# Performance work log

Measured on AMD Instinct MI355X. Metric: run time of the kernel, lower is better.

## Reference

```python
import jax, jax.numpy as jnp
import numpy as np


def avg_pool2(x):
    # 2x2 average pool, stride 2, NCHW
    b, c, h, w = x.shape
    return x.reshape(b, c, h // 2, 2, w // 2, 2).mean(axis=(3, 5))


def bisr_conv(x, W, mvk, mvb, beta):
    # ReDistribution: per-channel affine
    x = x * mvk + mvb
    # Spectral binary activation with tanh STE (forward value == sign(x))
    t = jnp.tanh(x * beta)
    xb = jax.lax.stop_gradient(jnp.sign(x)) - jax.lax.stop_gradient(t) + t
    # Binary weights: per-output-channel scale * sign(W), clipped-weight STE
    scale = jnp.mean(jnp.abs(W), axis=(1, 2, 3), keepdims=True)  # [O,1,1,1]
    bw_ng = jax.lax.stop_gradient(scale * jnp.sign(W))
    cw = jnp.clip(W, -1.0, 1.0)
    bw = bw_ng - jax.lax.stop_gradient(cw) + cw
    return jax.lax.conv_general_dilated(
        xb, bw, window_strides=(1, 1), padding=((1, 1), (1, 1)),
        dimension_numbers=('NCHW', 'OIHW', 'NCHW'))


def rprelu(x, pb0, alpha, pb1):
    x = x + pb0
    x = jnp.where(x >= 0, x, alpha * x)  # per-channel PReLU
    return x + pb1


def setup_inputs() -> dict:
    key = jax.random.key(0)
    B, C, H, W = 16, 128, 128, 128
    ks = jax.random.split(key, 3)
    x = jax.random.normal(ks[0], (B, C, H, W), dtype=jnp.float32)
    def branch_params(k):
        Wt = jax.random.normal(k, (C, C, 3, 3), dtype=jnp.float32) * 0.001
        return Wt
    zeros_c = jnp.zeros((1, C, 1, 1), jnp.float32)
    ones_c = jnp.ones((1, C, 1, 1), jnp.float32)
    alpha = jnp.full((1, C, 1, 1), 0.25, jnp.float32)
    return {
        'x': x,
        'W1': branch_params(ks[1]), 'mvk1': ones_c, 'mvb1': zeros_c,
        'beta1': jnp.ones((1,), jnp.float32), 'pb0_1': zeros_c,
        'alpha1': alpha, 'pb1_1': zeros_c,
        'W2': branch_params(ks[2]), 'mvk2': ones_c, 'mvb2': zeros_c,
        'beta2': jnp.ones((1,), jnp.float32), 'pb0_2': zeros_c,
        'alpha2': alpha, 'pb1_2': zeros_c,
    }


def reference(x, W1, mvk1, mvb1, beta1, pb0_1, alpha1, pb1_1,
              W2, mvk2, mvb2, beta2, pb0_2, alpha2, pb1_2):
    out = avg_pool2(x)  # [B, C, H/2, W/2]
    out1 = out + rprelu(bisr_conv(out, W1, mvk1, mvb1, beta1), pb0_1, alpha1, pb1_1)
    out2 = out + rprelu(bisr_conv(out, W2, mvk2, mvb2, beta2), pb0_2, alpha2, pb1_2)
    return jnp.concatenate([out1, out2], axis=1)  # [B, 2C, H/2, W/2]
```

## Files before the change

kernel.cpp:

```cpp
#include <hip/hip_runtime.h>
#include <stdint.h>

#define BATCH 16
#define CH    128
#define HIN   128
#define WIN   128
#define PH    64
#define PW    64

#define OFF_ABITS  16777216u
#define OFF_WBITS  18874368u
#define OFF_WSCALE 18911232u

typedef _Float16 half2v __attribute__((ext_vector_type(2)));

__global__ __launch_bounds__(256) void pool_pack(
    const float* __restrict__ x,
    const float* __restrict__ mvk1, const float* __restrict__ mvb1,
    const float* __restrict__ mvk2, const float* __restrict__ mvb2,
    _Float16* __restrict__ pooled, uint32_t* __restrict__ abits)
{
    __shared__ float spT[64][132];
    __shared__ float thrL[2][128];
    __shared__ uint32_t flipL[2][4];
    const int b  = blockIdx.y;
    const int ph = blockIdx.x;
    const int t  = threadIdx.x;

    {
        const int k31 = t & 31;
        const int c0  = (t >> 5) * 16;
        const int pw2 = k31 * 2;
        const float* xq = x + (((size_t)b * CH) * HIN + 2 * ph) * WIN + 4 * k31;
        for (int cg = 0; cg < 16; cg += 4) {
            float q0[4], q1[4];
            #pragma unroll
            for (int u = 0; u < 4; ++u) {
                const int c = c0 + cg + u;
                const float* xr = xq + (size_t)c * (HIN * WIN);
                const float4 r0 = *(const float4*)xr;
                const float4 r1 = *(const float4*)(xr + WIN);
                q0[u] = (r0.x + r0.y + r1.x + r1.y) * 0.25f;
                q1[u] = (r0.z + r0.w + r1.z + r1.w) * 0.25f;
                union { _Float16 h[2]; uint32_t w; } pk;
                pk.h[0] = (_Float16)q0[u];
                pk.h[1] = (_Float16)q1[u];
                *(uint32_t*)(pooled + ((size_t)(b * CH + c) * (PH * PW)) + ph * PW + pw2) = pk.w;
            }
            *(float4*)&spT[pw2][c0 + cg]     = make_float4(q0[0], q0[1], q0[2], q0[3]);
            *(float4*)&spT[pw2 + 1][c0 + cg] = make_float4(q1[0], q1[1], q1[2], q1[3]);
        }
    }

    {
        const int br = t >> 7, c = t & 127;
        const float kv = (br ? mvk2 : mvk1)[c];
        const float bv = (br ? mvb2 : mvb1)[c];
        float thr;
        if (kv != 0.0f) thr = -bv / kv;
        else thr = (bv < 0.0f) ? __builtin_inff() : -__builtin_inff();
        thrL[br][c] = thr;
        const unsigned long long bal = __ballot(kv < 0.0f);
        const int lane = t & 63;
        if (lane == 0)  flipL[br][c >> 5] = (uint32_t)bal;
        if (lane == 32) flipL[br][c >> 5] = (uint32_t)(bal >> 32);
    }
    __syncthreads();

    {
        const int wp = t & 1;
        const int pw = (t >> 1) & 63;
        const int br = t >> 7;
        const float4* prow = (const float4*)&spT[pw][wp * 64];
        const float4* trow = (const float4*)&thrL[br][wp * 64];
        uint32_t bits0 = 0, bits1 = 0;
        #pragma unroll
        for (int j4 = 0; j4 < 16; ++j4) {
            const float4 p  = prow[j4];
            const float4 tv = trow[j4];
            const uint32_t m = (uint32_t)(p.x < tv.x)
                             | ((uint32_t)(p.y < tv.y) << 1)
                             | ((uint32_t)(p.z < tv.z) << 2)
                             | ((uint32_t)(p.w < tv.w) << 3);
            if (j4 < 8) bits0 |= m << (j4 * 4);
            else        bits1 |= m << ((j4 - 8) * 4);
        }
        bits0 ^= flipL[br][wp * 2];
        bits1 ^= flipL[br][wp * 2 + 1];
        uint2* ab2 = (uint2*)abits;
        ab2[((size_t)(br * BATCH + b) * (PH * PW) + ph * PW + pw) * 2 + wp] =
            make_uint2(bits0, bits1);
    }
}

__global__ __launch_bounds__(64) void wprep(
    const float* __restrict__ W1, const float* __restrict__ W2,
    uint32_t* __restrict__ wbits, float* __restrict__ wscale)
{
    const int bo = blockIdx.x;
    const int branch = bo >> 7;
    const int o = bo & 127;
    const float* Wt = (branch ? W2 : W1) + (size_t)o * (CH * 9);
    const int t = threadIdx.x;

    float s = 0.f;
    for (int i = t; i < CH * 9; i += 64) s += fabsf(Wt[i]);
    #pragma unroll
    for (int off = 32; off >= 1; off >>= 1) s += __shfl_down(s, off);
    if (t == 0) wscale[bo] = s * (1.0f / (CH * 9));

    if (t < 36) {
        const int tap  = t >> 2;
        const int word = t & 3;
        uint32_t bits = 0;
        for (int j = 0; j < 32; ++j) {
            const int c = word * 32 + j;
            const float wv = Wt[c * 9 + tap];
            bits |= (wv < 0.0f ? 1u : 0u) << j;
        }
        wbits[(bo * 9 + tap) * 4 + word] = bits;
    }
}

__device__ __forceinline__ int popc4(uint4 a, uint4 w) {
    return __popc(a.x ^ w.x) + __popc(a.y ^ w.y) + __popc(a.z ^ w.z) + __popc(a.w ^ w.w);
}

__global__ __launch_bounds__(256, 8) void bconv_main(
    const uint32_t* __restrict__ abits_, const uint32_t* __restrict__ wbits_,
    const float* __restrict__ wscale, const _Float16* __restrict__ pooledH,
    const float* __restrict__ pb0_1, const float* __restrict__ alpha1, const float* __restrict__ pb1_1,
    const float* __restrict__ pb0_2, const float* __restrict__ alpha2, const float* __restrict__ pb1_2,
    float* __restrict__ out)
{
    __shared__ uint4 ha[10][66];
    const int bid = blockIdx.x;
    const int og     = bid & 7;
    const int ty     = (bid >> 3) & 7;
    const int b      = (bid >> 6) & 15;
    const int branch = bid >> 10;
    const int t  = threadIdx.x;
    const int cp = t & 31;
    const int r  = t >> 5;
    const int gr = ty * 8 + r;

    const uint4* ab = (const uint4*)abits_ + (size_t)(branch * BATCH + b) * (PH * PW);
    for (int e = t; e < 660; e += 256) {
        const int rr = e / 66, cc = e % 66;
        const int hp = ty * 8 - 1 + rr, wp = cc - 1;
        uint4 v = make_uint4(0u, 0u, 0u, 0u);
        if (hp >= 0 && hp < PH && wp >= 0 && wp < PW) v = ab[hp * PW + wp];
        ha[rr][cc] = v;
    }
    __syncthreads();

    uint4 a[3][4];
    #pragma unroll
    for (int i = 0; i < 3; ++i)
        #pragma unroll
        for (int j = 0; j < 4; ++j)
            a[i][j] = ha[r + i][2 * cp + j];

    const int mr0 = (gr > 0)  ? -1 : 0;
    const int mr2 = (gr < 63) ? -1 : 0;
    const int mcl = (cp > 0)  ? -1 : 0;
    const int mcr = (cp < 31) ? -1 : 0;
    const int rowsv = 1 + (gr > 0) + (gr < 63);
    const int base0 = 128 * rowsv * (2 + (cp > 0));
    const int base1 = 128 * rowsv * (2 + (cp < 31));

    const uint4* wb  = (const uint4*)wbits_ + (size_t)branch * (128 * 9);
    const float* wsv = wscale + branch * 128;
    const float* pb0 = branch ? pb0_2  : pb0_1;
    const float* alp = branch ? alpha2 : alpha1;
    const float* pb1 = branch ? pb1_2  : pb1_1;

    const _Float16* prow = pooledH + (size_t)(b * CH) * (PH * PW) + gr * PW + 2 * cp;
    float* orow = out + (size_t)(b * 2 * CH + branch * CH) * (PH * PW) + gr * PW + 2 * cp;

    const int o_beg = og * 16;
    for (int o = o_beg; o < o_beg + 16; ++o) {
        int pc0 = 0, pc1 = 0;
        #pragma unroll
        for (int dy = 0; dy < 3; ++dy) {
            const int mr = (dy == 0) ? mr0 : ((dy == 2) ? mr2 : -1);
            const uint4 w0 = wb[o * 9 + dy * 3 + 0];
            const uint4 w1 = wb[o * 9 + dy * 3 + 1];
            const uint4 w2 = wb[o * 9 + dy * 3 + 2];
            pc0 += popc4(a[dy][0], w0) & (mr & mcl);
            pc1 += popc4(a[dy][1], w0) & mr;
            pc0 += popc4(a[dy][1], w1) & mr;
            pc1 += popc4(a[dy][2], w1) & mr;
            pc0 += popc4(a[dy][2], w2) & mr;
            pc1 += popc4(a[dy][3], w2) & (mr & mcr);
        }
        const float sc = wsv[o], b0v = pb0[o], av = alp[o], b1v = pb1[o];
        float y0 = sc * (float)(base0 - 2 * pc0) + b0v;
        float y1 = sc * (float)(base1 - 2 * pc1) + b0v;
        y0 = fmaxf(y0, 0.f) + av * fminf(y0, 0.f) + b1v;
        y1 = fmaxf(y1, 0.f) + av * fminf(y1, 0.f) + b1v;
        const half2v pv = *(const half2v*)(prow + (size_t)o * (PH * PW));
        float2 st;
        st.x = (float)pv.x + y0;
        st.y = (float)pv.y + y1;
        *(float2*)(orow + (size_t)o * (PH * PW)) = st;
    }
}

extern "C" void kernel_launch(void* const* d_in, const int* in_sizes, int n_in,
                              void* d_out, int out_size, void* d_ws, size_t ws_size,
                              hipStream_t stream)
{
    const float* x      = (const float*)d_in[0];
    const float* W1     = (const float*)d_in[1];
    const float* mvk1   = (const float*)d_in[2];
    const float* mvb1   = (const float*)d_in[3];
    const float* pb0_1  = (const float*)d_in[5];
    const float* alpha1 = (const float*)d_in[6];
    const float* pb1_1  = (const float*)d_in[7];
    const float* W2     = (const float*)d_in[8];
    const float* mvk2   = (const float*)d_in[9];
    const float* mvb2   = (const float*)d_in[10];
    const float* pb0_2  = (const float*)d_in[12];
    const float* alpha2 = (const float*)d_in[13];
    const float* pb1_2  = (const float*)d_in[14];
    float* out = (float*)d_out;

    char* ws = (char*)d_ws;
    _Float16* pooled = (_Float16*)ws;
    uint32_t* abits  = (uint32_t*)(ws + OFF_ABITS);
    uint32_t* wbits  = (uint32_t*)(ws + OFF_WBITS);
    float*    wscale = (float*)(ws + OFF_WSCALE);

    hipLaunchKernelGGL(pool_pack, dim3(64, 16), dim3(256), 0, stream,
                       x, mvk1, mvb1, mvk2, mvb2, pooled, abits);
    hipLaunchKernelGGL(wprep, dim3(256), dim3(64), 0, stream, W1, W2, wbits, wscale);
    hipLaunchKernelGGL(bconv_main, dim3(2048), dim3(256), 0, stream,
                       abits, wbits, wscale, pooled,
                       pb0_1, alpha1, pb1_1, pb0_2, alpha2, pb1_2, out);
}
```

Measured before the change: 295.8 us.

## Replace border masking with precomputed weight corrections and fuse accumulate popcount

The binary conv inner loop no longer masks popcounts at image borders. Zero-padded activation bits read as +1 there, so wprep now precomputes per-output-channel edge sums of the weight signs, and a few conditional integer adds in the epilogue remove that contribution. Popcounts use v_bcnt_u32_b32 with a built-in accumulator to save add instructions. pool_pack now computes sign bits directly with an fma compare while pooling, replacing the shared float transpose and threshold stage, and wprep is launched first. The cost is extra workspace and epilogue loads per output channel, plus a small change in how zero-scale channels are handled.

Result: faster. 289.8 us (-2.0%).

```diff
diff --git a/kernel.cpp b/kernel.cpp
--- a/kernel.cpp
+++ b/kernel.cpp
@@ -11,6 +11,7 @@
 #define OFF_ABITS  16777216u
 #define OFF_WBITS  18874368u
 #define OFF_WSCALE 18911232u
+#define OFF_WCORR  18912256u
 
 typedef _Float16 half2v __attribute__((ext_vector_type(2)));
 
@@ -20,83 +21,68 @@
     const float* __restrict__ mvk2, const float* __restrict__ mvb2,
     _Float16* __restrict__ pooled, uint32_t* __restrict__ abits)
 {
-    __shared__ float spT[64][132];
-    __shared__ float thrL[2][128];
-    __shared__ uint32_t flipL[2][4];
+    __shared__ float kL[2][128], bL[2][128];
+    __shared__ unsigned short sb[2][64][8];
     const int b  = blockIdx.y;
     const int ph = blockIdx.x;
     const int t  = threadIdx.x;
 
     {
-        const int k31 = t & 31;
-        const int c0  = (t >> 5) * 16;
-        const int pw2 = k31 * 2;
-        const float* xq = x + (((size_t)b * CH) * HIN + 2 * ph) * WIN + 4 * k31;
-        for (int cg = 0; cg < 16; cg += 4) {
-            float q0[4], q1[4];
-            #pragma unroll
-            for (int u = 0; u < 4; ++u) {
-                const int c = c0 + cg + u;
-                const float* xr = xq + (size_t)c * (HIN * WIN);
-                const float4 r0 = *(const float4*)xr;
-                const float4 r1 = *(const float4*)(xr + WIN);
-                q0[u] = (r0.x + r0.y + r1.x + r1.y) * 0.25f;
-                q1[u] = (r0.z + r0.w + r1.z + r1.w) * 0.25f;
-                union { _Float16 h[2]; uint32_t w; } pk;
-                pk.h[0] = (_Float16)q0[u];
-                pk.h[1] = (_Float16)q1[u];
-                *(uint32_t*)(pooled + ((size_t)(b * CH + c) * (PH * PW)) + ph * PW + pw2) = pk.w;
-            }
-            *(float4*)&spT[pw2][c0 + cg]     = make_float4(q0[0], q0[1], q0[2], q0[3]);
-            *(float4*)&spT[pw2 + 1][c0 + cg] = make_float4(q1[0], q1[1], q1[2], q1[3]);
-        }
-    }
-
-    {
         const int br = t >> 7, c = t & 127;
-        const float kv = (br ? mvk2 : mvk1)[c];
-        const float bv = (br ? mvb2 : mvb1)[c];
-        float thr;
-        if (kv != 0.0f) thr = -bv / kv;
-        else thr = (bv < 0.0f) ? __builtin_inff() : -__builtin_inff();
-        thrL[br][c] = thr;
-        const unsigned long long bal = __ballot(kv < 0.0f);
-        const int lane = t & 63;
-        if (lane == 0)  flipL[br][c >> 5] = (uint32_t)bal;
-        if (lane == 32) flipL[br][c >> 5] = (uint32_t)(bal >> 32);
-    }
+        kL[br][c] = (br ? mvk2 : mvk1)[c];
+        bL[br][c] = (br ? mvb2 : mvb1)[c];
+    }
+    __syncthreads();
+
+    const int k31 = t & 31;
+    const int g   = t >> 5;
+    const int pw2 = 2 * k31;
+    const float* xq = x + (((size_t)b * CH) * HIN + 2 * ph) * WIN + 4 * k31;
+    uint32_t m00 = 0, m01 = 0, m10 = 0, m11 = 0;
+    #pragma unroll
+    for (int u = 0; u < 16; ++u) {
+        const int c = g * 16 + u;
+        const float* xr = xq + (size_t)c * (HIN * WIN);
+        const float4 r0 = *(const float4*)xr;
+        const float4 r1 = *(const float4*)(xr + WIN);
+        const float q0 = (r0.x + r0.y + r1.x + r1.y) * 0.25f;
+        const float q1 = (r0.z + r0.w + r1.z + r1.w) * 0.25f;
+        union { _Float16 h[2]; uint32_t w; } pk;
+        pk.h[0] = (_Float16)q0;
+        pk.h[1] = (_Float16)q1;
+        *(uint32_t*)(pooled + ((size_t)(b * CH + c) * (PH * PW)) + ph * PW + pw2) = pk.w;
+        const float k0 = kL[0][c], b0 = bL[0][c];
+        const float k1 = kL[1][c], b1 = bL[1][c];
+        m00 |= (uint32_t)(fmaf(q0, k0, b0) < 0.0f) << u;
+        m01 |= (uint32_t)(fmaf(q1, k0, b0) < 0.0f) << u;
+        m10 |= (uint32_t)(fmaf(q0, k1, b1) < 0.0f) << u;
+        m11 |= (uint32_t)(fmaf(q1, k1, b1) < 0.0f) << u;
+    }
+    sb[0][pw2][g]     = (unsigned short)m00;
+    sb[0][pw2 + 1][g] = (unsigned short)m01;
+    sb[1][pw2][g]     = (unsigned short)m10;
+    sb[1][pw2 + 1][g] = (unsigned short)m11;
     __syncthreads();
 
     {
         const int wp = t & 1;
-        const int pw = (t >> 1) & 63;
+        const int px = (t >> 1) & 63;
         const int br = t >> 7;
-        const float4* prow = (const float4*)&spT[pw][wp * 64];
-        const float4* trow = (const float4*)&thrL[br][wp * 64];
-        uint32_t bits0 = 0, bits1 = 0;
-        #pragma unroll
-        for (int j4 = 0; j4 < 16; ++j4) {
-            const float4 p  = prow[j4];
-            const float4 tv = trow[j4];
-            const uint32_t m = (uint32_t)(p.x < tv.x)
-                             | ((uint32_t)(p.y < tv.y) << 1)
-                             | ((uint32_t)(p.z < tv.z) << 2)
-                             | ((uint32_t)(p.w < tv.w) << 3);
-            if (j4 < 8) bits0 |= m << (j4 * 4);
-            else        bits1 |= m << ((j4 - 8) * 4);
-        }
-        bits0 ^= flipL[br][wp * 2];
-        bits1 ^= flipL[br][wp * 2 + 1];
-        uint2* ab2 = (uint2*)abits;
-        ab2[((size_t)(br * BATCH + b) * (PH * PW) + ph * PW + pw) * 2 + wp] =
-            make_uint2(bits0, bits1);
+        const unsigned short* h = &sb[br][px][wp * 4];
+        uint2 v;
+        v.x = (uint32_t)h[0] | ((uint32_t)h[1] << 16);
+        v.y = (uint32_t)h[2] | ((uint32_t)h[3] << 16);
+        ((uint2*)abits)[((size_t)(br * BATCH + b) * (PH * PW) + ph * PW + px) * 2 + wp] = v;
     }
 }
 
 __global__ __launch_bounds__(64) void wprep(
     const float* __restrict__ W1, const float* __restrict__ W2,
-    uint32_t* __restrict__ wbits, float* __restrict__ wscale)
-{
+    uint32_t* __restrict__ wbits, float* __restrict__ wscale,
+    int* __restrict__ wcorr)
+{
+    __shared__ uint32_t swb[9][4];
+    __shared__ int tpv[9];
     const int bo = blockIdx.x;
     const int branch = bo >> 7;
     const int o = bo & 127;
@@ -114,21 +100,47 @@
         const int word = t & 3;
         uint32_t bits = 0;
         for (int j = 0; j < 32; ++j) {
-            const int c = word * 32 + j;
-            const float wv = Wt[c * 9 + tap];
+            const float wv = Wt[(word * 32 + j) * 9 + tap];
             bits |= (wv < 0.0f ? 1u : 0u) << j;
         }
         wbits[(bo * 9 + tap) * 4 + word] = bits;
-    }
-}
-
-__device__ __forceinline__ int popc4(uint4 a, uint4 w) {
-    return __popc(a.x ^ w.x) + __popc(a.y ^ w.y) + __popc(a.z ^ w.z) + __popc(a.w ^ w.w);
+        swb[tap][word] = bits;
+    }
+    __syncthreads();
+    if (t < 9)
+        tpv[t] = 2 * (__popc(swb[t][0]) + __popc(swb[t][1]) +
+                      __popc(swb[t][2]) + __popc(swb[t][3])) - 128;
+    __syncthreads();
+    if (t == 0) {
+        int* wc = wcorr + bo * 8;
+        wc[0] = tpv[0] + tpv[1] + tpv[2];
+        wc[1] = tpv[6] + tpv[7] + tpv[8];
+        wc[2] = tpv[0] + tpv[3] + tpv[6];
+        wc[3] = tpv[2] + tpv[5] + tpv[8];
+        wc[4] = tpv[0];
+        wc[5] = tpv[2];
+        wc[6] = tpv[6];
+        wc[7] = tpv[8];
+    }
+}
+
+__device__ __forceinline__ int bcnt_acc(uint32_t xv, int acc) {
+    int d;
+    asm("v_bcnt_u32_b32 %0, %1, %2" : "=v"(d) : "v"(xv), "v"(acc));
+    return d;
+}
+__device__ __forceinline__ int xacc4(uint4 a, uint4 w, int acc) {
+    acc = bcnt_acc(a.x ^ w.x, acc);
+    acc = bcnt_acc(a.y ^ w.y, acc);
+    acc = bcnt_acc(a.z ^ w.z, acc);
+    acc = bcnt_acc(a.w ^ w.w, acc);
+    return acc;
 }
 
 __global__ __launch_bounds__(256, 8) void bconv_main(
     const uint32_t* __restrict__ abits_, const uint32_t* __restrict__ wbits_,
-    const float* __restrict__ wscale, const _Float16* __restrict__ pooledH,
+    const float* __restrict__ wscale, const int* __restrict__ wcorr,
+    const _Float16* __restrict__ pooledH,
     const float* __restrict__ pb0_1, const float* __restrict__ alpha1, const float* __restrict__ pb1_1,
     const float* __restrict__ pb0_2, const float* __restrict__ alpha2, const float* __restrict__ pb1_2,
     float* __restrict__ out)
@@ -161,15 +173,11 @@
         for (int j = 0; j < 4; ++j)
             a[i][j] = ha[r + i][2 * cp + j];
 
-    const int mr0 = (gr > 0)  ? -1 : 0;
-    const int mr2 = (gr < 63) ? -1 : 0;
-    const int mcl = (cp > 0)  ? -1 : 0;
-    const int mcr = (cp < 31) ? -1 : 0;
-    const int rowsv = 1 + (gr > 0) + (gr < 63);
-    const int base0 = 128 * rowsv * (2 + (cp > 0));
-    const int base1 = 128 * rowsv * (2 + (cp < 31));
+    const bool fr0 = (gr == 0), fr2 = (gr == 63);
+    const bool fc0 = (cp == 0), fc2 = (cp == 31);
 
     const uint4* wb  = (const uint4*)wbits_ + (size_t)branch * (128 * 9);
+    const int*   wcb = wcorr + branch * (128 * 8);
     const float* wsv = wscale + branch * 128;
     const float* pb0 = branch ? pb0_2  : pb0_1;
     const float* alp = branch ? alpha2 : alpha1;
@@ -183,20 +191,27 @@
         int pc0 = 0, pc1 = 0;
         #pragma unroll
         for (int dy = 0; dy < 3; ++dy) {
-            const int mr = (dy == 0) ? mr0 : ((dy == 2) ? mr2 : -1);
             const uint4 w0 = wb[o * 9 + dy * 3 + 0];
             const uint4 w1 = wb[o * 9 + dy * 3 + 1];
             const uint4 w2 = wb[o * 9 + dy * 3 + 2];
-            pc0 += popc4(a[dy][0], w0) & (mr & mcl);
-            pc1 += popc4(a[dy][1], w0) & mr;
-            pc0 += popc4(a[dy][1], w1) & mr;
-            pc1 += popc4(a[dy][2], w1) & mr;
-            pc0 += popc4(a[dy][2], w2) & mr;
-            pc1 += popc4(a[dy][3], w2) & (mr & mcr);
+            pc0 = xacc4(a[dy][0], w0, pc0);
+            pc1 = xacc4(a[dy][1], w0, pc1);
+            pc0 = xacc4(a[dy][1], w1, pc0);
+            pc1 = xacc4(a[dy][2], w1, pc1);
+            pc0 = xacc4(a[dy][2], w2, pc0);
+            pc1 = xacc4(a[dy][3], w2, pc1);
         }
+        const int4 wcA = *(const int4*)(wcb + o * 8);
+        const int4 wcB = *(const int4*)(wcb + o * 8 + 4);
+        const int baser = (fr0 ? wcA.x : 0) + (fr2 ? wcA.y : 0);
+        const int cc0e  = wcA.z - (fr0 ? wcB.x : 0) - (fr2 ? wcB.z : 0);
+        const int cc2e  = wcA.w - (fr0 ? wcB.y : 0) - (fr2 ? wcB.w : 0);
+        const int S0 = 1152 + baser + (fc0 ? cc0e : 0) - 2 * pc0;
+        const int S1 = 1152 + baser + (fc2 ? cc2e : 0) - 2 * pc1;
+
         const float sc = wsv[o], b0v = pb0[o], av = alp[o], b1v = pb1[o];
-        float y0 = sc * (float)(base0 - 2 * pc0) + b0v;
-        float y1 = sc * (float)(base1 - 2 * pc1) + b0v;
+        float y0 = sc * (float)S0 + b0v;
+        float y1 = sc * (float)S1 + b0v;
         y0 = fmaxf(y0, 0.f) + av * fminf(y0, 0.f) + b1v;
         y1 = fmaxf(y1, 0.f) + av * fminf(y1, 0.f) + b1v;
         const half2v pv = *(const half2v*)(prow + (size_t)o * (PH * PW));
@@ -231,11 +246,12 @@
     uint32_t* abits  = (uint32_t*)(ws + OFF_ABITS);
     uint32_t* wbits  = (uint32_t*)(ws + OFF_WBITS);
     float*    wscale = (float*)(ws + OFF_WSCALE);
-
+    int*      wcorr  = (int*)(ws + OFF_WCORR);
+
+    hipLaunchKernelGGL(wprep, dim3(256), dim3(64), 0, stream, W1, W2, wbits, wscale, wcorr);
     hipLaunchKernelGGL(pool_pack, dim3(64, 16), dim3(256), 0, stream,
                        x, mvk1, mvb1, mvk2, mvb2, pooled, abits);
-    hipLaunchKernelGGL(wprep, dim3(256), dim3(64), 0, stream, W1, W2, wbits, wscale);
     hipLaunchKernelGGL(bconv_main, dim3(2048), dim3(256), 0, stream,
-                       abits, wbits, wscale, pooled,
+                       abits, wbits, wscale, wcorr, pooled,
                        pb0_1, alpha1, pb1_1, pb0_2, alpha2, pb1_2, out);
 }
```
